# Kernel optimization log

Measured on AMD Instinct MI355X. Metric: run time of the kernel, lower is better.

## Reference

```python
import jax, jax.numpy as jnp
import numpy as np
from jax import lax

C = 512          # in_channels
L = 4            # fcos_conv_layers
NUM_CLS = 1      # fcos_num_class - 1
PRIOR_BIAS = float(-np.log((1 - 0.01) / 0.01))
BN_EPS = 1e-5


def conv1d(x, w, b, pad):
    # x: [B, Cin, T], w: [Cout, Cin, K]
    y = lax.conv_general_dilated(x, w, window_strides=(1,), padding=[(pad, pad)],
                                 dimension_numbers=('NCH', 'OIH', 'NCH'))
    return y + b[None, :, None]


def bn(x, g, b, m, v):
    inv = lax.rsqrt(v + BN_EPS)
    return (x - m[None, :, None]) * (g * inv)[None, :, None] + b[None, :, None]


def tower(x, ws, bs, gs, bes, ms, vs):
    # ws: [L, C, C, 3]; fixed small loop over layers
    for i in range(L):
        x = jax.nn.relu(bn(conv1d(x, ws[i], bs[i], 1), gs[i], bes[i], ms[i], vs[i]))
    return x


def setup_inputs() -> dict:
    key = jax.random.key(0)
    ks = jax.random.split(key, 32)
    d = {}
    d['f0'] = jax.random.normal(ks[0], (8, C, 1024), jnp.float32)
    d['f1'] = jax.random.normal(ks[1], (8, C, 512), jnp.float32)
    d['f2'] = jax.random.normal(ks[2], (8, C, 256), jnp.float32)

    def nrm(k, shape):
        return 0.01 * jax.random.normal(k, shape, jnp.float32)

    # cls / bbox towers: stacked conv + BN params
    d['cls_tw_w'] = nrm(ks[3], (L, C, C, 3)); d['cls_tw_b'] = jnp.zeros((L, C))
    d['cls_bn_g'] = jnp.ones((L, C)); d['cls_bn_b'] = jnp.zeros((L, C))
    d['cls_bn_m'] = jnp.zeros((L, C)); d['cls_bn_v'] = jnp.ones((L, C))
    d['box_tw_w'] = nrm(ks[4], (L, C, C, 3)); d['box_tw_b'] = jnp.zeros((L, C))
    d['box_bn_g'] = jnp.ones((L, C)); d['box_bn_b'] = jnp.zeros((L, C))
    d['box_bn_m'] = jnp.zeros((L, C)); d['box_bn_v'] = jnp.ones((L, C))

    d['logits_w'] = nrm(ks[5], (NUM_CLS, C, 3))
    d['logits_b'] = jnp.full((NUM_CLS,), PRIOR_BIAS, jnp.float32)
    d['bbox_w'] = nrm(ks[6], (2, C, 3)); d['bbox_b'] = jnp.zeros((2,))

    d['mix_w'] = nrm(ks[7], (C, 2 * C, 1)); d['mix_b'] = jnp.zeros((C,))
    d['mix_bn_g'] = jnp.ones((C,)); d['mix_bn_b'] = jnp.zeros((C,))
    d['mix_bn_m'] = jnp.zeros((C,)); d['mix_bn_v'] = jnp.ones((C,))

    d['iou_w1'] = nrm(ks[8], (C // 2, C, 3)); d['iou_b1'] = jnp.zeros((C // 2,))
    d['iou_bn_g'] = jnp.ones((C // 2,)); d['iou_bn_b'] = jnp.zeros((C // 2,))
    d['iou_bn_m'] = jnp.zeros((C // 2,)); d['iou_bn_v'] = jnp.ones((C // 2,))
    d['iou_w2'] = nrm(ks[9], (1, C // 2, 1)); d['iou_b2'] = jnp.zeros((1,))

    d['scales'] = jnp.ones((3,), jnp.float32)
    return d


def reference(f0, f1, f2,
              cls_tw_w, cls_tw_b, cls_bn_g, cls_bn_b, cls_bn_m, cls_bn_v,
              box_tw_w, box_tw_b, box_bn_g, box_bn_b, box_bn_m, box_bn_v,
              logits_w, logits_b, bbox_w, bbox_b,
              mix_w, mix_b, mix_bn_g, mix_bn_b, mix_bn_m, mix_bn_v,
              iou_w1, iou_b1, iou_bn_g, iou_bn_b, iou_bn_m, iou_bn_v,
              iou_w2, iou_b2, scales):
    outs = []
    for l, x in enumerate([f0, f1, f2]):
        ct = tower(x, cls_tw_w, cls_tw_b, cls_bn_g, cls_bn_b, cls_bn_m, cls_bn_v)
        bt = tower(x, box_tw_w, box_tw_b, box_bn_g, box_bn_b, box_bn_m, box_bn_v)
        logits = conv1d(ct, logits_w, logits_b, 1)                      # [B, 1, T]
        bbox = jnp.exp(conv1d(bt, bbox_w, bbox_b, 1) * scales[l])       # [B, 2, T]
        mix = jax.nn.relu(bn(conv1d(jnp.concatenate([ct, bt], axis=1), mix_w, mix_b, 0),
                             mix_bn_g, mix_bn_b, mix_bn_m, mix_bn_v))   # [B, C, T]
        h = jax.nn.relu(bn(conv1d(mix, iou_w1, iou_b1, 1),
                           iou_bn_g, iou_bn_b, iou_bn_m, iou_bn_v))
        iou = conv1d(h, iou_w2, iou_b2, 0)                              # [B, 1, T]
        outs.append(jnp.concatenate([logits, bbox, iou], axis=1))       # [B, 4, T]
    return jnp.concatenate(outs, axis=-1)  # [B, 4, T0+T1+T2]
```

## Files before the change

### kernel.cpp

```cpp
#include <hip/hip_runtime.h>
#include <hip/hip_bf16.h>


typedef __bf16 bf16x8 __attribute__((ext_vector_type(8)));
typedef float f32x4 __attribute__((ext_vector_type(4)));

__device__ __forceinline__ float bf2f(unsigned short u) {
    union { unsigned int i; float f; } c; c.i = ((unsigned int)u) << 16; return c.f;
}
__device__ __forceinline__ unsigned short f2bf(float f) {
    union { __hip_bfloat16 h; unsigned short u; } c; c.h = __float2bfloat16(f); return c.u;
}

__device__ __forceinline__ void gload16(const void* g, void* l) {
    __builtin_amdgcn_global_load_lds(
        (const __attribute__((address_space(1))) unsigned int*)g,
        (__attribute__((address_space(3))) unsigned int*)l,
        16, 0, 0);
}

__global__ __launch_bounds__(512, 2)
void conv_tower(const unsigned short* __restrict__ X, int xstride, int ci_twstride,
                const unsigned short* __restrict__ W,
                const float* __restrict__ Bs,
                unsigned short* __restrict__ Y)
{
    __shared__ alignas(16) unsigned short Xb[2][17 * 512];
    __shared__ alignas(16) unsigned short Wb[3][16 * 512];

    const int L = blockIdx.x;
    const int P = (L & 7) * 28 + (L >> 3);
    const int tt = P >> 2, sub = P & 3;
    const int tw = sub >> 1, co0 = (sub & 1) << 8;

    int rowstart;
    if (tt < 32)      { rowstart = (tt >> 2) * 1026 + 1 + ((tt & 3) << 8); }
    else if (tt < 48) { int i = tt - 32; rowstart = 8208 + (i >> 1) * 514 + 1 + ((i & 1) << 8); }
    else              { rowstart = 12320 + (tt - 48) * 258 + 1; }

    const int tid = threadIdx.x;
    const int lane = tid & 63, wid = tid >> 6;
    const int wco = (wid >> 2) << 7;
    const int wt  = (wid & 3) << 6;
    const int lr = lane & 15;
    const int sr = lane >> 4;

    const unsigned short* Wp = W + (size_t)tw * 3145728;
    const float* Bp = Bs + tw * 2048;
    const int co_out0 = tw * 512 + co0;
    const int ci_off = tw * ci_twstride;

    const unsigned short* xga[3]; unsigned short* xl[3];
#pragma unroll
    for (int p = 0; p < 3; ++p) {
        int seg = (p < 2) ? (p * 8 + wid) : 16;
        xl[p] = (unsigned short*)Xb[0] + seg * 512;
        int g = seg * 64 + lane;
        int row = g >> 2, sc = (g & 3) ^ ((row >> 1) & 3);
        xga[p] = X + (size_t)(rowstart - 1 + row) * xstride + ci_off + sc * 8;
    }
    const unsigned short* wga[2]; unsigned short* wl[2];
#pragma unroll
    for (int p = 0; p < 2; ++p) {
        int seg = p * 8 + wid;
        wl[p] = (unsigned short*)Wb[0] + seg * 512;
        int g = seg * 64 + lane;
        int row = g >> 2, sc = (g & 3) ^ ((row >> 1) & 3);
        wga[p] = Wp + (size_t)(co0 + row) * 1536 + sc * 8;
    }
    constexpr int XBSZ = 17 * 512;
    constexpr int WBSZ = 16 * 512;

    int aoff[8];
#pragma unroll
    for (int mi = 0; mi < 8; ++mi) {
        int ra = wco + mi * 16 + lr;
        aoff[mi] = ra * 64 + (((sr ^ (ra >> 1)) & 3) << 4);
    }
    int boff[3][4];
#pragma unroll
    for (int kk = 0; kk < 3; ++kk)
#pragma unroll
        for (int ni = 0; ni < 4; ++ni) {
            int rb = wt + ni * 16 + lr + kk;
            boff[kk][ni] = rb * 64 + (((sr ^ (rb >> 1)) & 3) << 4);
        }

    f32x4 acc[8][4];
#pragma unroll
    for (int i = 0; i < 8; ++i)
#pragma unroll
        for (int j = 0; j < 4; ++j) acc[i][j] = (f32x4){0.f, 0.f, 0.f, 0.f};

#pragma unroll
    for (int p = 0; p < 3; ++p) gload16(xga[p], xl[p]);
#pragma unroll
    for (int p = 0; p < 2; ++p) {
        gload16(wga[p],       wl[p]);
        gload16(wga[p] + 512, wl[p] + WBSZ);
    }
    asm volatile("s_waitcnt vmcnt(0)" ::: "memory");
    __builtin_amdgcn_s_barrier();

    bf16x8 af[2][8], bv[2][4];
#pragma unroll
    for (int mi = 0; mi < 8; ++mi) af[0][mi] = *(const bf16x8*)((const char*)Wb[0] + aoff[mi]);
#pragma unroll
    for (int ni = 0; ni < 4; ++ni) bv[0][ni] = *(const bf16x8*)((const char*)Xb[0] + boff[0][ni]);

#pragma unroll
    for (int s = 0; s < 48; ++s) {
        const int cr = s & 1, nx = cr ^ 1;
        const int ks = s / 3;
        if (s < 46) {
            const int sp = s + 2;
            const int tap2 = sp % 3, ks2 = sp / 3;
#pragma unroll
            for (int p = 0; p < 2; ++p)
                gload16(wga[p] + tap2 * 512 + ks2 * 32, wl[p] + (sp % 3) * WBSZ);
        }
        if ((s % 3) == 0 && ks < 15) {
#pragma unroll
            for (int p = 0; p < 3; ++p)
                gload16(xga[p] + (ks + 1) * 32, xl[p] + ((ks + 1) & 1) * XBSZ);
        }
        if (s < 47) {
            const int sn = s + 1;
            const int tapn = sn % 3, wbn = sn % 3, xbn = (sn / 3) & 1;
#pragma unroll
            for (int mi = 0; mi < 8; ++mi)
                af[nx][mi] = *(const bf16x8*)((const char*)Wb[wbn] + aoff[mi]);
#pragma unroll
            for (int ni = 0; ni < 4; ++ni)
                bv[nx][ni] = *(const bf16x8*)((const char*)Xb[xbn] + boff[tapn][ni]);
        }
        __builtin_amdgcn_sched_barrier(0);
        __builtin_amdgcn_s_setprio(1);
#pragma unroll
        for (int mi = 0; mi < 8; ++mi)
#pragma unroll
            for (int ni = 0; ni < 4; ++ni)
                acc[mi][ni] = __builtin_amdgcn_mfma_f32_16x16x32_bf16(af[cr][mi], bv[cr][ni], acc[mi][ni], 0, 0, 0);
        __builtin_amdgcn_s_setprio(0);
        asm volatile("s_waitcnt vmcnt(0)" ::: "memory");
        __builtin_amdgcn_s_barrier();
    }

    const int r4 = sr * 4;
#pragma unroll
    for (int mi = 0; mi < 8; ++mi) {
        int co_l = wco + mi * 16 + r4;
        float b0 = Bp[co0 + co_l + 0], b1 = Bp[co0 + co_l + 1];
        float b2 = Bp[co0 + co_l + 2], b3 = Bp[co0 + co_l + 3];
#pragma unroll
        for (int ni = 0; ni < 4; ++ni) {
            int t = wt + ni * 16 + lr;
            f32x4 a = acc[mi][ni];
            float v0 = fmaxf(a[0] + b0, 0.f), v1 = fmaxf(a[1] + b1, 0.f);
            float v2 = fmaxf(a[2] + b2, 0.f), v3 = fmaxf(a[3] + b3, 0.f);
            union { unsigned long long u; unsigned short s[4]; } pk;
            pk.s[0] = f2bf(v0); pk.s[1] = f2bf(v1); pk.s[2] = f2bf(v2); pk.s[3] = f2bf(v3);
            *(unsigned long long*)(Y + (size_t)(rowstart + t) * 1024 + co_out0 + co_l) = pk.u;
        }
    }
}

__device__ __forceinline__ void tile_decode(int ct, int& rowstart, int& t0, int& Tl) {
    if (ct < 64)      { Tl = 1024; int b = ct >> 3;                 t0 = (ct & 7) << 7; rowstart = b * 1026 + 1; }
    else if (ct < 96) { Tl = 512;  int i = ct - 64; int b = i >> 2; t0 = (i & 3) << 7; rowstart = 8208 + b * 514 + 1; }
    else              { Tl = 256;  int i = ct - 96; int b = i >> 1; t0 = (i & 1) << 7; rowstart = 12320 + b * 258 + 1; }
}

template<int KSIZE>
__global__ __launch_bounds__(256)
void conv_gemm(const unsigned short* __restrict__ X, int xstride, int ci0_base, int ci_twstride, int Cin,
               const unsigned short* __restrict__ W, int w_twstride,
               const float* __restrict__ Bs, int b_twstride,
               unsigned short* __restrict__ Y, int ystride, int co_twstride,
               int relu)
{
    constexpr int BM = 128, BN = 128, BK = 32;
    constexpr int NR = BN + KSIZE - 1;
    constexpr int XSEG = (NR * 64 + 1023) / 1024;
    constexpr int XPW  = (XSEG + 3) / 4;
    constexpr int WSEG = KSIZE * BM * 64 / 1024;
    constexpr int WPW  = WSEG / 4;
    __shared__ alignas(16) unsigned short Xs[2 * XSEG * 512];
    __shared__ alignas(16) unsigned short Ws[2 * WSEG * 512];

    const int tid = threadIdx.x;
    const int lane = tid & 63, wid = tid >> 6;
    int rowstart, t0, Tl;
    tile_decode(blockIdx.x, rowstart, t0, Tl);
    const int co0 = blockIdx.y * BM;
    const int tw = blockIdx.z;
    const int ci_off = ci0_base + tw * ci_twstride;
    const unsigned short* Wp = W + (size_t)tw * w_twstride;
    const float* Bp = Bs + tw * b_twstride;
    const int co_out0 = tw * co_twstride + co0;

    const int wm = (wid >> 1) * 64, wn = (wid & 1) * 64;
    const int lr = lane & 15;
    const int sr = lane >> 4;

    const unsigned short* xga[XPW]; unsigned short* xl[XPW];
#pragma unroll
    for (int p = 0; p < XPW; ++p) {
        int seg = (KSIZE == 3) ? ((p < 2) ? p * 4 + wid : 8) : (p * 4 + wid);
        xl[p] = Xs + seg * 512;
        int g = seg * 64 + lane;
        int row = g >> 2, s = (g & 3) ^ ((row >> 1) & 3);
        xga[p] = X + (size_t)(rowstart - (KSIZE >> 1) + row) * xstride + ci_off + s * 8;
    }
    const unsigned short* wga[WPW]; unsigned short* wl[WPW];
#pragma unroll
    for (int p = 0; p < WPW; ++p) {
        int seg = p * 4 + wid;
        wl[p] = Ws + seg * 512;
        int g = seg * 64 + lane;
        int row = g >> 2, s = (g & 3) ^ ((row >> 1) & 3);
        int co = row & (BM - 1), kk = row >> 7;
        wga[p] = Wp + (size_t)(co0 + co) * (KSIZE * Cin) + kk * Cin + s * 8;
    }

    f32x4 acc[4][4];
#pragma unroll
    for (int i = 0; i < 4; ++i)
#pragma unroll
        for (int j = 0; j < 4; ++j) acc[i][j] = (f32x4){0.f, 0.f, 0.f, 0.f};

    auto STAGE = [&](int buf) {
#pragma unroll
        for (int p = 0; p < XPW; ++p) { gload16(xga[p], xl[p] + buf * (XSEG * 512)); xga[p] += BK; }
#pragma unroll
        for (int p = 0; p < WPW; ++p) { gload16(wga[p], wl[p] + buf * (WSEG * 512)); wga[p] += BK; }
    };

    const int nk = Cin / BK;
    STAGE(0);
    int cur = 0;
    for (int ks = 0; ks < nk; ++ks) {
        if (ks + 1 < nk) {
            STAGE(cur ^ 1);
            if constexpr (KSIZE == 3) asm volatile("s_waitcnt vmcnt(9)" ::: "memory");
            else                      asm volatile("s_waitcnt vmcnt(4)" ::: "memory");
        } else {
            asm volatile("s_waitcnt vmcnt(0)" ::: "memory");
        }
        __builtin_amdgcn_sched_barrier(0);
        __builtin_amdgcn_s_barrier();

        const char* bXs = (const char*)Xs + cur * (XSEG * 1024);
        const char* bWs = (const char*)Ws + cur * (WSEG * 1024);
#pragma unroll
        for (int kk = 0; kk < KSIZE; ++kk) {
            bf16x8 af[4], bv[4];
#pragma unroll
            for (int mi = 0; mi < 4; ++mi) {
                int ra = kk * BM + wm + mi * 16 + lr;
                af[mi] = *(const bf16x8*)(bWs + ra * 64 + (((sr ^ (ra >> 1)) & 3) << 4));
                int rb = wn + mi * 16 + lr + kk;
                bv[mi] = *(const bf16x8*)(bXs + rb * 64 + (((sr ^ (rb >> 1)) & 3) << 4));
            }
#pragma unroll
            for (int mi = 0; mi < 4; ++mi)
#pragma unroll
                for (int ni = 0; ni < 4; ++ni)
                    acc[mi][ni] = __builtin_amdgcn_mfma_f32_16x16x32_bf16(af[mi], bv[ni], acc[mi][ni], 0, 0, 0);
        }
        __builtin_amdgcn_sched_barrier(0);
        __builtin_amdgcn_s_barrier();
        cur ^= 1;
    }

    const int r4 = (lane >> 4) * 4;
#pragma unroll
    for (int mi = 0; mi < 4; ++mi) {
        int co_l = wm + mi * 16 + r4;
        float b0 = Bp[co0 + co_l + 0], b1 = Bp[co0 + co_l + 1];
        float b2 = Bp[co0 + co_l + 2], b3 = Bp[co0 + co_l + 3];
#pragma unroll
        for (int ni = 0; ni < 4; ++ni) {
            int t = t0 + wn + ni * 16 + lr;
            f32x4 a = acc[mi][ni];
            float v0 = a[0] + b0, v1 = a[1] + b1, v2 = a[2] + b2, v3 = a[3] + b3;
            if (relu) {
                v0 = fmaxf(v0, 0.f); v1 = fmaxf(v1, 0.f);
                v2 = fmaxf(v2, 0.f); v3 = fmaxf(v3, 0.f);
            }
            union { unsigned long long u; unsigned short s[4]; } pk;
            pk.s[0] = f2bf(v0); pk.s[1] = f2bf(v1); pk.s[2] = f2bf(v2); pk.s[3] = f2bf(v3);
            *(unsigned long long*)(Y + (size_t)(rowstart + t) * ystride + co_out0 + co_l) = pk.u;
        }
    }
}

__global__ __launch_bounds__(256)
void zero_pads(unsigned short* __restrict__ act0, unsigned short* __restrict__ catA,
               unsigned short* __restrict__ catB, unsigned short* __restrict__ mixo,
               unsigned short* __restrict__ iouh)
{
    int c = blockIdx.x >> 1, side = blockIdx.x & 1;
    int start, Tl;
    if (c < 8)       { start = c * 1026;               Tl = 1024; }
    else if (c < 16) { start = 8208 + (c - 8) * 514;   Tl = 512;  }
    else             { start = 12320 + (c - 16) * 258; Tl = 256;  }
    size_t prow = start + (side ? Tl + 1 : 0);
    int tid = threadIdx.x;
    uint4 z = make_uint4(0u, 0u, 0u, 0u);
    if (tid < 64)  *(uint4*)(act0 + prow * 512 + tid * 8) = z;
    if (tid < 128) { *(uint4*)(catA + prow * 1024 + tid * 8) = z;
                     *(uint4*)(catB + prow * 1024 + tid * 8) = z; }
    if (tid >= 128 && tid < 192) *(uint4*)(mixo + prow * 512 + (tid - 128) * 8) = z;
    if (tid >= 192 && tid < 224) *(uint4*)(iouh + prow * 256 + (tid - 192) * 8) = z;
}

__global__ __launch_bounds__(256)
void transpose_in(const float* __restrict__ f0, const float* __restrict__ f1, const float* __restrict__ f2,
                  unsigned short* __restrict__ act0)
{
    __shared__ float tile[32][33];
    int bx = blockIdx.x;
    const float* src; int Tl, padbase, b, t0;
    if (bx < 256)      { src = f0; Tl = 1024; int i = bx;       b = i >> 5; t0 = (i & 31) << 5; padbase = b * 1026; }
    else if (bx < 384) { src = f1; Tl = 512;  int i = bx - 256; b = i >> 4; t0 = (i & 15) << 5; padbase = 8208 + b * 514; }
    else               { src = f2; Tl = 256;  int i = bx - 384; b = i >> 3; t0 = (i & 7)  << 5; padbase = 12320 + b * 258; }
    int c0 = blockIdx.y << 5;
    const float* sb = src + (size_t)b * 512 * Tl;
    int tl = threadIdx.x & 31, cl = threadIdx.x >> 5;
#pragma unroll
    for (int j = 0; j < 4; ++j) {
        int c = cl + j * 8;
        tile[c][tl] = sb[(size_t)(c0 + c) * Tl + t0 + tl];
    }
    __syncthreads();
    int cc = threadIdx.x & 31, tr0 = threadIdx.x >> 5;
    size_t base = (size_t)(padbase + 1 + t0) * 512 + c0;
#pragma unroll
    for (int j = 0; j < 4; ++j) {
        int tr = tr0 + j * 8;
        act0[base + (size_t)tr * 512 + cc] = f2bf(tile[cc][tr]);
    }
}

__global__ __launch_bounds__(256)
void prep_tower(const float* __restrict__ cls_w, const float* __restrict__ box_w,
                const float* __restrict__ cg, const float* __restrict__ cvv,
                const float* __restrict__ bg, const float* __restrict__ bvv,
                unsigned short* __restrict__ Wt)
{
    int idx = blockIdx.x * 256 + threadIdx.x;
    if (idx >= 2 * 4 * 512 * 3 * 512) return;
    int ci = idx & 511;
    int kk = (idx >> 9) % 3;
    int co = (idx / 1536) & 511;
    int l  = (idx / 786432) & 3;
    int tw = idx / 3145728;
    const float* w = tw ? box_w : cls_w;
    const float* g = tw ? bg : cg;
    const float* v = tw ? bvv : cvv;
    float s = g[l * 512 + co] * rsqrtf(v[l * 512 + co] + 1e-5f);
    float val = w[(((size_t)(l * 512 + co)) * 512 + ci) * 3 + kk] * s;
    Wt[idx] = f2bf(val);
}

__global__ __launch_bounds__(256)
void prep_misc(const float* mix_w, const float* mix_b, const float* mg, const float* mbeta, const float* mm, const float* mv,
               const float* iou_w1, const float* iou_b1, const float* ig, const float* ibeta, const float* im, const float* iv,
               const float* cls_b, const float* cg, const float* cbeta, const float* cm, const float* cv2,
               const float* box_b, const float* bg, const float* bbeta, const float* bm, const float* bv2,
               unsigned short* Wmix, unsigned short* Wiou, float* Bt, float* Bmix, float* Biou)
{
    int idx = blockIdx.x * 256 + threadIdx.x;
    if (idx < 524288) {
        int co = idx >> 10;
        float s = mg[co] * rsqrtf(mv[co] + 1e-5f);
        Wmix[idx] = f2bf(mix_w[idx] * s);
        return;
    }
    idx -= 524288;
    if (idx < 393216) {
        int ci = idx & 511, kk = (idx >> 9) % 3, co = idx / 1536;
        float s = ig[co] * rsqrtf(iv[co] + 1e-5f);
        Wiou[idx] = f2bf(iou_w1[((size_t)(co * 512 + ci)) * 3 + kk] * s);
        return;
    }
    idx -= 393216;
    if (idx < 4096) {
        int co = idx & 511, l = (idx >> 9) & 3, tw = idx >> 11;
        const float* g = tw ? bg : cg; const float* v = tw ? bv2 : cv2;
        const float* m = tw ? bm : cm; const float* be = tw ? bbeta : cbeta;
        const float* cb = tw ? box_b : cls_b;
        int o = l * 512 + co;
        float s = g[o] * rsqrtf(v[o] + 1e-5f);
        Bt[idx] = (cb[o] - m[o]) * s + be[o];
        return;
    }
    idx -= 4096;
    if (idx < 512) {
        float s = mg[idx] * rsqrtf(mv[idx] + 1e-5f);
        Bmix[idx] = (mix_b[idx] - mm[idx]) * s + mbeta[idx];
        return;
    }
    idx -= 512;
    if (idx < 256) {
        float s = ig[idx] * rsqrtf(iv[idx] + 1e-5f);
        Biou[idx] = (iou_b1[idx] - im[idx]) * s + ibeta[idx];
    }
}

__global__ __launch_bounds__(256)
void heads_kernel(const unsigned short* __restrict__ catb, const unsigned short* __restrict__ iouh,
                  const float* __restrict__ lw, const float* __restrict__ lb,
                  const float* __restrict__ bw, const float* __restrict__ bb,
                  const float* __restrict__ iw, const float* __restrict__ ib,
                  const float* __restrict__ scales, float* __restrict__ out)
{
    const int lane = threadIdx.x & 63;
    const int wid = threadIdx.x >> 6;

    float lwr[24], bwr0[24], bwr1[24], iwr[4];
    {
        const float4* p = (const float4*)(lw + lane * 24);
#pragma unroll
        for (int q = 0; q < 6; ++q) {
            float4 v = p[q];
            lwr[q * 4 + 0] = v.x; lwr[q * 4 + 1] = v.y; lwr[q * 4 + 2] = v.z; lwr[q * 4 + 3] = v.w;
        }
        p = (const float4*)(bw + lane * 24);
#pragma unroll
        for (int q = 0; q < 6; ++q) {
            float4 v = p[q];
            bwr0[q * 4 + 0] = v.x; bwr0[q * 4 + 1] = v.y; bwr0[q * 4 + 2] = v.z; bwr0[q * 4 + 3] = v.w;
        }
        p = (const float4*)(bw + 1536 + lane * 24);
#pragma unroll
        for (int q = 0; q < 6; ++q) {
            float4 v = p[q];
            bwr1[q * 4 + 0] = v.x; bwr1[q * 4 + 1] = v.y; bwr1[q * 4 + 2] = v.z; bwr1[q * 4 + 3] = v.w;
        }
        float4 v = *(const float4*)(iw + lane * 4);
        iwr[0] = v.x; iwr[1] = v.y; iwr[2] = v.z; iwr[3] = v.w;
    }
    const float lb0 = lb[0], bb0 = bb[0], bb1 = bb[1], ib0 = ib[0];
    const float s0 = scales[0], s1 = scales[1], s2 = scales[2];

    for (int r = blockIdx.x * 4 + wid; r < 14336; r += gridDim.x * 4) {
        int tlog, roff, tgoff, padbase; float sc;
        if (r < 8192)       { tlog = 10; roff = 0;     tgoff = 0;    sc = s0; }
        else if (r < 12288) { tlog = 9;  roff = 8192;  tgoff = 1024; sc = s1; }
        else                { tlog = 8;  roff = 12288; tgoff = 1536; sc = s2; }
        int i = r - roff;
        int Tl = 1 << tlog;
        int b = i >> tlog, t = i & (Tl - 1);
        if (r < 8192)       padbase = b * 1026;
        else if (r < 12288) padbase = 8208 + b * 514;
        else                padbase = 12320 + b * 258;
        int prow = padbase + 1 + t;

        float al = 0.f, a0 = 0.f, a1 = 0.f, ai = 0.f;
        const unsigned short* base = catb + (size_t)prow * 1024 + lane * 8;
#pragma unroll
        for (int kk = 0; kk < 3; ++kk) {
            union { uint4 u; unsigned short s[8]; } cv, bvv;
            cv.u = *(const uint4*)(base + (kk - 1) * 1024);
            bvv.u = *(const uint4*)(base + (kk - 1) * 1024 + 512);
#pragma unroll
            for (int j = 0; j < 8; ++j) {
                float xc = bf2f(cv.s[j]);
                float xb = bf2f(bvv.s[j]);
                al = fmaf(xc, lwr[j * 3 + kk], al);
                a0 = fmaf(xb, bwr0[j * 3 + kk], a0);
                a1 = fmaf(xb, bwr1[j * 3 + kk], a1);
            }
        }
        {
            union { uint2 u; unsigned short s[4]; } hv;
            hv.u = *(const uint2*)(iouh + (size_t)prow * 256 + lane * 4);
#pragma unroll
            for (int j = 0; j < 4; ++j) ai = fmaf(bf2f(hv.s[j]), iwr[j], ai);
        }
#pragma unroll
        for (int off = 32; off > 0; off >>= 1) {
            al += __shfl_xor(al, off);
            a0 += __shfl_xor(a0, off);
            a1 += __shfl_xor(a1, off);
            ai += __shfl_xor(ai, off);
        }
        if (lane == 0) {
            int tg = tgoff + t;
            out[((size_t)b * 4 + 0) * 1792 + tg] = al + lb0;
            out[((size_t)b * 4 + 1) * 1792 + tg] = expf((a0 + bb0) * sc);
            out[((size_t)b * 4 + 2) * 1792 + tg] = expf((a1 + bb1) * sc);
            out[((size_t)b * 4 + 3) * 1792 + tg] = ai + ib0;
        }
    }
}

extern "C" void kernel_launch(void* const* d_in, const int* in_sizes, int n_in,
                              void* d_out, int out_size, void* d_ws, size_t ws_size,
                              hipStream_t stream)
{
    const float* f0       = (const float*)d_in[0];
    const float* f1       = (const float*)d_in[1];
    const float* f2       = (const float*)d_in[2];
    const float* cls_tw_w = (const float*)d_in[3];
    const float* cls_tw_b = (const float*)d_in[4];
    const float* cls_bn_g = (const float*)d_in[5];
    const float* cls_bn_b = (const float*)d_in[6];
    const float* cls_bn_m = (const float*)d_in[7];
    const float* cls_bn_v = (const float*)d_in[8];
    const float* box_tw_w = (const float*)d_in[9];
    const float* box_tw_b = (const float*)d_in[10];
    const float* box_bn_g = (const float*)d_in[11];
    const float* box_bn_b = (const float*)d_in[12];
    const float* box_bn_m = (const float*)d_in[13];
    const float* box_bn_v = (const float*)d_in[14];
    const float* logits_w = (const float*)d_in[15];
    const float* logits_b = (const float*)d_in[16];
    const float* bbox_w   = (const float*)d_in[17];
    const float* bbox_b   = (const float*)d_in[18];
    const float* mix_w    = (const float*)d_in[19];
    const float* mix_b    = (const float*)d_in[20];
    const float* mix_bn_g = (const float*)d_in[21];
    const float* mix_bn_b = (const float*)d_in[22];
    const float* mix_bn_m = (const float*)d_in[23];
    const float* mix_bn_v = (const float*)d_in[24];
    const float* iou_w1   = (const float*)d_in[25];
    const float* iou_b1   = (const float*)d_in[26];
    const float* iou_bn_g = (const float*)d_in[27];
    const float* iou_bn_b = (const float*)d_in[28];
    const float* iou_bn_m = (const float*)d_in[29];
    const float* iou_bn_v = (const float*)d_in[30];
    const float* iou_w2   = (const float*)d_in[31];
    const float* iou_b2   = (const float*)d_in[32];
    const float* scales   = (const float*)d_in[33];

    unsigned char* ws = (unsigned char*)d_ws;
    unsigned short* Wt   = (unsigned short*)(ws + 0);
    unsigned short* Wmix = (unsigned short*)(ws + 12582912);
    unsigned short* Wiou = (unsigned short*)(ws + 13631488);
    float*          Bt   = (float*)(ws + 14417920);
    float*          Bmix = (float*)(ws + 14434304);
    float*          Biou = (float*)(ws + 14436352);
    unsigned short* act0 = (unsigned short*)(ws + 14437376);
    unsigned short* catA = (unsigned short*)(ws + 29182976);
    unsigned short* catB = (unsigned short*)(ws + 58674176);
    unsigned short* mixo = (unsigned short*)(ws + 88165376);
    unsigned short* iouh = (unsigned short*)(ws + 102910976);

    zero_pads<<<dim3(48), dim3(256), 0, stream>>>(act0, catA, catB, mixo, iouh);
    prep_tower<<<dim3(24576), dim3(256), 0, stream>>>(cls_tw_w, box_tw_w, cls_bn_g, cls_bn_v,
                                                      box_bn_g, box_bn_v, Wt);
    prep_misc<<<dim3(3603), dim3(256), 0, stream>>>(mix_w, mix_b, mix_bn_g, mix_bn_b, mix_bn_m, mix_bn_v,
                                                    iou_w1, iou_b1, iou_bn_g, iou_bn_b, iou_bn_m, iou_bn_v,
                                                    cls_tw_b, cls_bn_g, cls_bn_b, cls_bn_m, cls_bn_v,
                                                    box_tw_b, box_bn_g, box_bn_b, box_bn_m, box_bn_v,
                                                    Wmix, Wiou, Bt, Bmix, Biou);
    transpose_in<<<dim3(448, 16), dim3(256), 0, stream>>>(f0, f1, f2, act0);

    conv_tower<<<dim3(224), dim3(512), 0, stream>>>(act0, 512, 0,   Wt,            Bt,        catA);
    conv_tower<<<dim3(224), dim3(512), 0, stream>>>(catA, 1024, 512, Wt + 786432,  Bt + 512,  catB);
    conv_tower<<<dim3(224), dim3(512), 0, stream>>>(catB, 1024, 512, Wt + 1572864, Bt + 1024, catA);
    conv_tower<<<dim3(224), dim3(512), 0, stream>>>(catA, 1024, 512, Wt + 2359296, Bt + 1536, catB);
    conv_gemm<1><<<dim3(112, 4, 1), 256, 0, stream>>>(catB, 1024, 0, 0, 1024,
                                                      Wmix, 0, Bmix, 0, mixo, 512, 0, 1);
    conv_gemm<3><<<dim3(112, 2, 1), 256, 0, stream>>>(mixo, 512, 0, 0, 512,
                                                      Wiou, 0, Biou, 0, iouh, 256, 0, 1);
    heads_kernel<<<dim3(896), dim3(256), 0, stream>>>(catB, iouh, logits_w, logits_b,
                                                      bbox_w, bbox_b, iou_w2, iou_b2, scales,
                                                      (float*)d_out);
}
```

Measured before the change: 298.3 us.

## Shrink conv tower tiles to 128 timesteps with 256-thread blocks and tap-wise pipeline

Reworks the tower conv kernel so each block covers 256 output channels by 128 timesteps with 4 waves instead of 256 by 256 with 8 waves, doubling the grid to 448 blocks. The K loop is restructured to process one input-channel chunk per iteration with three tap sub-steps, double-buffering weights per tap and X per chunk, and it waits on LDS reads before issuing MFMAs. The aim is better CU occupancy and load balance, since 224 blocks underfill the GPU, at the cost of more weight traffic per output and more barriers. The original conv_tower is left with a broken buffer indexing expression and is no longer called. A fixed copy, conv_tower_fixed, is launched instead.

New measurement: 310.4 us. 4.1% more time.

```diff
diff --git a/kernel.cpp b/kernel.cpp
--- a/kernel.cpp
+++ b/kernel.cpp
@@ -19,31 +19,36 @@
         16, 0, 0);
 }
 
-__global__ __launch_bounds__(512, 2)
+__device__ __forceinline__ void tile_decode(int ct, int& rowstart, int& t0, int& Tl) {
+    if (ct < 64)      { Tl = 1024; int b = ct >> 3;                 t0 = (ct & 7) << 7; rowstart = b * 1026 + 1; }
+    else if (ct < 96) { Tl = 512;  int i = ct - 64; int b = i >> 2; t0 = (i & 3) << 7; rowstart = 8208 + b * 514 + 1; }
+    else              { Tl = 256;  int i = ct - 96; int b = i >> 1; t0 = (i & 1) << 7; rowstart = 12320 + b * 258 + 1; }
+}
+
+__global__ __launch_bounds__(256, 2)
 void conv_tower(const unsigned short* __restrict__ X, int xstride, int ci_twstride,
                 const unsigned short* __restrict__ W,
                 const float* __restrict__ Bs,
                 unsigned short* __restrict__ Y)
 {
-    __shared__ alignas(16) unsigned short Xb[2][17 * 512];
-    __shared__ alignas(16) unsigned short Wb[3][16 * 512];
+    __shared__ alignas(16) unsigned short Xb[2][9 * 512];
+    __shared__ alignas(16) unsigned short Wb[2][16 * 512];
+    constexpr int XBSZ = 9 * 512;
+    constexpr int WBSZ = 16 * 512;
 
     const int L = blockIdx.x;
-    const int P = (L & 7) * 28 + (L >> 3);
-    const int tt = P >> 2, sub = P & 3;
+    const int P = (L & 7) * 56 + (L >> 3);
+    const int ct = P >> 2, sub = P & 3;
     const int tw = sub >> 1, co0 = (sub & 1) << 8;
 
-    int rowstart;
-    if (tt < 32)      { rowstart = (tt >> 2) * 1026 + 1 + ((tt & 3) << 8); }
-    else if (tt < 48) { int i = tt - 32; rowstart = 8208 + (i >> 1) * 514 + 1 + ((i & 1) << 8); }
-    else              { rowstart = 12320 + (tt - 48) * 258 + 1; }
-
-    const int tid = threadIdx.x;
-    const int lane = tid & 63, wid = tid >> 6;
-    const int wco = (wid >> 2) << 7;
-    const int wt  = (wid & 3) << 6;
-    const int lr = lane & 15;
-    const int sr = lane >> 4;
+    int rowstart, t0, Tl;
+    tile_decode(ct, rowstart, t0, Tl);
+    const int rtile = rowstart + t0;
+
+    const int tid = threadIdx.x, lane = tid & 63, wid = tid >> 6;
+    const int wco = (wid >> 1) << 7;
+    const int wt  = (wid & 1) << 6;
+    const int lr = lane & 15, sr = lane >> 4;
 
     const unsigned short* Wp = W + (size_t)tw * 3145728;
     const float* Bp = Bs + tw * 2048;
@@ -53,23 +58,21 @@
     const unsigned short* xga[3]; unsigned short* xl[3];
 #pragma unroll
     for (int p = 0; p < 3; ++p) {
-        int seg = (p < 2) ? (p * 8 + wid) : 16;
+        int seg = (p < 2) ? (p * 4 + wid) : 8;
         xl[p] = (unsigned short*)Xb[0] + seg * 512;
-        int g = seg * 64 + lane;
-        int row = g >> 2, sc = (g & 3) ^ ((row >> 1) & 3);
-        xga[p] = X + (size_t)(rowstart - 1 + row) * xstride + ci_off + sc * 8;
-    }
-    const unsigned short* wga[2]; unsigned short* wl[2];
-#pragma unroll
-    for (int p = 0; p < 2; ++p) {
-        int seg = p * 8 + wid;
+        int row = seg * 16 + (lane >> 2);
+        int sc = (lane & 3) ^ ((row >> 1) & 3);
+        xga[p] = X + (size_t)(rtile - 1 + row) * xstride + ci_off + sc * 8;
+    }
+    const unsigned short* wga[4]; unsigned short* wl[4];
+#pragma unroll
+    for (int p = 0; p < 4; ++p) {
+        int seg = p * 4 + wid;
         wl[p] = (unsigned short*)Wb[0] + seg * 512;
-        int g = seg * 64 + lane;
-        int row = g >> 2, sc = (g & 3) ^ ((row >> 1) & 3);
+        int row = seg * 16 + (lane >> 2);
+        int sc = (lane & 3) ^ ((row >> 1) & 3);
         wga[p] = Wp + (size_t)(co0 + row) * 1536 + sc * 8;
     }
-    constexpr int XBSZ = 17 * 512;
-    constexpr int WBSZ = 16 * 512;
 
     int aoff[8];
 #pragma unroll
@@ -95,55 +98,49 @@
 #pragma unroll
     for (int p = 0; p < 3; ++p) gload16(xga[p], xl[p]);
 #pragma unroll
-    for (int p = 0; p < 2; ++p) {
-        gload16(wga[p],       wl[p]);
-        gload16(wga[p] + 512, wl[p] + WBSZ);
-    }
+    for (int p = 0; p < 4; ++p) gload16(wga[p], wl[p]);
     asm volatile("s_waitcnt vmcnt(0)" ::: "memory");
     __builtin_amdgcn_s_barrier();
 
-    bf16x8 af[2][8], bv[2][4];
-#pragma unroll
-    for (int mi = 0; mi < 8; ++mi) af[0][mi] = *(const bf16x8*)((const char*)Wb[0] + aoff[mi]);
-#pragma unroll
-    for (int ni = 0; ni < 4; ++ni) bv[0][ni] = *(const bf16x8*)((const char*)Xb[0] + boff[0][ni]);
-
-#pragma unroll
-    for (int s = 0; s < 48; ++s) {
-        const int cr = s & 1, nx = cr ^ 1;
-        const int ks = s / 3;
-        if (s < 46) {
-            const int sp = s + 2;
-            const int tap2 = sp % 3, ks2 = sp / 3;
-#pragma unroll
-            for (int p = 0; p < 2; ++p)
-                gload16(wga[p] + tap2 * 512 + ks2 * 32, wl[p] + (sp % 3) * WBSZ);
-        }
-        if ((s % 3) == 0 && ks < 15) {
-#pragma unroll
-            for (int p = 0; p < 3; ++p)
-                gload16(xga[p] + (ks + 1) * 32, xl[p] + ((ks + 1) & 1) * XBSZ);
-        }
-        if (s < 47) {
-            const int sn = s + 1;
-            const int tapn = sn % 3, wbn = sn % 3, xbn = (sn / 3) & 1;
+    for (int ks = 0; ks < 16; ++ks) {
+        const int pk = ks & 1, po = pk ^ 1;
+        const char* Xcur = (const char*)Xb[0] + pk * (XBSZ * 2);
+        const char* Wpk  = (const char*)Wb[0] + pk * (WBSZ * 2);
+        const char* Wpo  = (const char*)Wb[0] + po * (WBSZ * 2);
+
+        auto TAP = [&](const char* wbuf, int kk) {
+            bf16x8 af[8], bv[4];
 #pragma unroll
             for (int mi = 0; mi < 8; ++mi)
-                af[nx][mi] = *(const bf16x8*)((const char*)Wb[wbn] + aoff[mi]);
+                af[mi] = *(const bf16x8*)(wbuf + aoff[mi]);
 #pragma unroll
             for (int ni = 0; ni < 4; ++ni)
-                bv[nx][ni] = *(const bf16x8*)((const char*)Xb[xbn] + boff[tapn][ni]);
-        }
-        __builtin_amdgcn_sched_barrier(0);
-        __builtin_amdgcn_s_setprio(1);
-#pragma unroll
-        for (int mi = 0; mi < 8; ++mi)
-#pragma unroll
-            for (int ni = 0; ni < 4; ++ni)
-                acc[mi][ni] = __builtin_amdgcn_mfma_f32_16x16x32_bf16(af[cr][mi], bv[cr][ni], acc[mi][ni], 0, 0, 0);
-        __builtin_amdgcn_s_setprio(0);
-        asm volatile("s_waitcnt vmcnt(0)" ::: "memory");
-        __builtin_amdgcn_s_barrier();
+                bv[ni] = *(const bf16x8*)(Xcur + boff[kk][ni]);
+            asm volatile("s_waitcnt lgkmcnt(0)" ::: "memory");
+            __builtin_amdgcn_sched_barrier(0);
+            __builtin_amdgcn_s_setprio(1);
+#pragma unroll
+            for (int mi = 0; mi < 8; ++mi)
+#pragma unroll
+                for (int ni = 0; ni < 4; ++ni)
+                    acc[mi][ni] = __builtin_amdgcn_mfma_f32_16x16x32_bf16(af[mi], bv[ni], acc[mi][ni], 0, 0, 0);
+            __builtin_amdgcn_s_setprio(0);
+            asm volatile("s_waitcnt vmcnt(0)" ::: "memory");
+            __builtin_amdgcn_s_barrier();
+        };
+
+#pragma unroll
+        for (int p = 0; p < 4; ++p) gload16(wga[p] + 512 + ks * 32, wl[p] + po * (WBSZ * 1) + po * 0 + po * WBSZ - po * WBSZ + po * WBSZ);
+        ;
+        TAP(Wpk, 0);
+#pragma unroll
+        for (int p = 0; p < 4; ++p) gload16(wga[p] + 1024 + ks * 32, wl[p] + pk * WBSZ);
+        TAP(Wpo, 1);
+        if (ks < 15) {
+#pragma unroll
+            for (int p = 0; p < 4; ++p) gload16(wga[p] + (ks + 1) * 32, wl[p] + po * WBSZ);
+        }
+        TAP(Wpk, 2);
     }
 
     const int r4 = sr * 4;
@@ -158,17 +155,151 @@
             f32x4 a = acc[mi][ni];
             float v0 = fmaxf(a[0] + b0, 0.f), v1 = fmaxf(a[1] + b1, 0.f);
             float v2 = fmaxf(a[2] + b2, 0.f), v3 = fmaxf(a[3] + b3, 0.f);
-            union { unsigned long long u; unsigned short s[4]; } pk;
-            pk.s[0] = f2bf(v0); pk.s[1] = f2bf(v1); pk.s[2] = f2bf(v2); pk.s[3] = f2bf(v3);
-            *(unsigned long long*)(Y + (size_t)(rowstart + t) * 1024 + co_out0 + co_l) = pk.u;
-        }
-    }
-}
-
-__device__ __forceinline__ void tile_decode(int ct, int& rowstart, int& t0, int& Tl) {
-    if (ct < 64)      { Tl = 1024; int b = ct >> 3;                 t0 = (ct & 7) << 7; rowstart = b * 1026 + 1; }
-    else if (ct < 96) { Tl = 512;  int i = ct - 64; int b = i >> 2; t0 = (i & 3) << 7; rowstart = 8208 + b * 514 + 1; }
-    else              { Tl = 256;  int i = ct - 96; int b = i >> 1; t0 = (i & 1) << 7; rowstart = 12320 + b * 258 + 1; }
+            union { unsigned long long u; unsigned short s[4]; } pk2;
+            pk2.s[0] = f2bf(v0); pk2.s[1] = f2bf(v1); pk2.s[2] = f2bf(v2); pk2.s[3] = f2bf(v3);
+            *(unsigned long long*)(Y + (size_t)(rtile + t) * 1024 + co_out0 + co_l) = pk2.u;
+        }
+    }
+}
+
+__global__ __launch_bounds__(256, 2)
+void conv_tower_fixed(const unsigned short* __restrict__ X, int xstride, int ci_twstride,
+                      const unsigned short* __restrict__ W,
+                      const float* __restrict__ Bs,
+                      unsigned short* __restrict__ Y)
+{
+    __shared__ alignas(16) unsigned short Xb[2][9 * 512];
+    __shared__ alignas(16) unsigned short Wb[2][16 * 512];
+    constexpr int XBSZ = 9 * 512;
+    constexpr int WBSZ = 16 * 512;
+
+    const int L = blockIdx.x;
+    const int P = (L & 7) * 56 + (L >> 3);
+    const int ct = P >> 2, sub = P & 3;
+    const int tw = sub >> 1, co0 = (sub & 1) << 8;
+
+    int rowstart, t0, Tl;
+    tile_decode(ct, rowstart, t0, Tl);
+    const int rtile = rowstart + t0;
+
+    const int tid = threadIdx.x, lane = tid & 63, wid = tid >> 6;
+    const int wco = (wid >> 1) << 7;
+    const int wt  = (wid & 1) << 6;
+    const int lr = lane & 15, sr = lane >> 4;
+
+    const unsigned short* Wp = W + (size_t)tw * 3145728;
+    const float* Bp = Bs + tw * 2048;
+    const int co_out0 = tw * 512 + co0;
+    const int ci_off = tw * ci_twstride;
+
+    const unsigned short* xga[3]; unsigned short* xl[3];
+#pragma unroll
+    for (int p = 0; p < 3; ++p) {
+        int seg = (p < 2) ? (p * 4 + wid) : 8;
+        xl[p] = (unsigned short*)Xb[0] + seg * 512;
+        int row = seg * 16 + (lane >> 2);
+        int sc = (lane & 3) ^ ((row >> 1) & 3);
+        xga[p] = X + (size_t)(rtile - 1 + row) * xstride + ci_off + sc * 8;
+    }
+    const unsigned short* wga[4]; unsigned short* wl[4];
+#pragma unroll
+    for (int p = 0; p < 4; ++p) {
+        int seg = p * 4 + wid;
+        wl[p] = (unsigned short*)Wb[0] + seg * 512;
+        int row = seg * 16 + (lane >> 2);
+        int sc = (lane & 3) ^ ((row >> 1) & 3);
+        wga[p] = Wp + (size_t)(co0 + row) * 1536 + sc * 8;
+    }
+
+    int aoff[8];
+#pragma unroll
+    for (int mi = 0; mi < 8; ++mi) {
+        int ra = wco + mi * 16 + lr;
+        aoff[mi] = ra * 64 + (((sr ^ (ra >> 1)) & 3) << 4);
+    }
+    int boff[3][4];
+#pragma unroll
+    for (int kk = 0; kk < 3; ++kk)
+#pragma unroll
+        for (int ni = 0; ni < 4; ++ni) {
+            int rb = wt + ni * 16 + lr + kk;
+            boff[kk][ni] = rb * 64 + (((sr ^ (rb >> 1)) & 3) << 4);
+        }
+
+    f32x4 acc[8][4];
+#pragma unroll
+    for (int i = 0; i < 8; ++i)
+#pragma unroll
+        for (int j = 0; j < 4; ++j) acc[i][j] = (f32x4){0.f, 0.f, 0.f, 0.f};
+
+#pragma unroll
+    for (int p = 0; p < 3; ++p) gload16(xga[p], xl[p]);
+#pragma unroll
+    for (int p = 0; p < 4; ++p) gload16(wga[p], wl[p]);
+    asm volatile("s_waitcnt vmcnt(0)" ::: "memory");
+    __builtin_amdgcn_s_barrier();
+
+    for (int ks = 0; ks < 16; ++ks) {
+        const int pk = ks & 1, po = pk ^ 1;
+        const char* Xcur = (const char*)Xb[0] + pk * (XBSZ * 2);
+        const char* Wpk  = (const char*)Wb[0] + pk * (WBSZ * 2);
+        const char* Wpo  = (const char*)Wb[0] + po * (WBSZ * 2);
+
+        auto TAP = [&](const char* wbuf, int kk) {
+            bf16x8 af[8], bv[4];
+#pragma unroll
+            for (int mi = 0; mi < 8; ++mi)
+                af[mi] = *(const bf16x8*)(wbuf + aoff[mi]);
+#pragma unroll
+            for (int ni = 0; ni < 4; ++ni)
+                bv[ni] = *(const bf16x8*)(Xcur + boff[kk][ni]);
+            asm volatile("s_waitcnt lgkmcnt(0)" ::: "memory");
+            __builtin_amdgcn_sched_barrier(0);
+            __builtin_amdgcn_s_setprio(1);
+#pragma unroll
+            for (int mi = 0; mi < 8; ++mi)
+#pragma unroll
+                for (int ni = 0; ni < 4; ++ni)
+                    acc[mi][ni] = __builtin_amdgcn_mfma_f32_16x16x32_bf16(af[mi], bv[ni], acc[mi][ni], 0, 0, 0);
+            __builtin_amdgcn_s_setprio(0);
+            asm volatile("s_waitcnt vmcnt(0)" ::: "memory");
+            __builtin_amdgcn_s_barrier();
+        };
+
+#pragma unroll
+        for (int p = 0; p < 4; ++p) gload16(wga[p] + 512 + ks * 32, wl[p] + po * WBSZ);
+        if (ks < 15) {
+#pragma unroll
+            for (int p = 0; p < 3; ++p) gload16(xga[p] + (ks + 1) * 32, xl[p] + po * XBSZ);
+        }
+        TAP(Wpk, 0);
+#pragma unroll
+        for (int p = 0; p < 4; ++p) gload16(wga[p] + 1024 + ks * 32, wl[p] + pk * WBSZ);
+        TAP(Wpo, 1);
+        if (ks < 15) {
+#pragma unroll
+            for (int p = 0; p < 4; ++p) gload16(wga[p] + (ks + 1) * 32, wl[p] + po * WBSZ);
+        }
+        TAP(Wpk, 2);
+    }
+
+    const int r4 = sr * 4;
+#pragma unroll
+    for (int mi = 0; mi < 8; ++mi) {
+        int co_l = wco + mi * 16 + r4;
+        float b0 = Bp[co0 + co_l + 0], b1 = Bp[co0 + co_l + 1];
+        float b2 = Bp[co0 + co_l + 2], b3 = Bp[co0 + co_l + 3];
+#pragma unroll
+        for (int ni = 0; ni < 4; ++ni) {
+            int t = wt + ni * 16 + lr;
+            f32x4 a = acc[mi][ni];
+            float v0 = fmaxf(a[0] + b0, 0.f), v1 = fmaxf(a[1] + b1, 0.f);
+            float v2 = fmaxf(a[2] + b2, 0.f), v3 = fmaxf(a[3] + b3, 0.f);
+            union { unsigned long long u; unsigned short s[4]; } pk2;
+            pk2.s[0] = f2bf(v0); pk2.s[1] = f2bf(v1); pk2.s[2] = f2bf(v2); pk2.s[3] = f2bf(v3);
+            *(unsigned long long*)(Y + (size_t)(rtile + t) * 1024 + co_out0 + co_l) = pk2.u;
+        }
+    }
 }
 
 template<int KSIZE>
@@ -210,7 +341,7 @@
         xl[p] = Xs + seg * 512;
         int g = seg * 64 + lane;
         int row = g >> 2, s = (g & 3) ^ ((row >> 1) & 3);
-        xga[p] = X + (size_t)(rowstart - (KSIZE >> 1) + row) * xstride + ci_off + s * 8;
+        xga[p] = X + (size_t)(rowstart + t0 - (KSIZE >> 1) + row) * xstride + ci_off + s * 8;
     }
     const unsigned short* wga[WPW]; unsigned short* wl[WPW];
 #pragma unroll
@@ -559,10 +690,10 @@
                                                     Wmix, Wiou, Bt, Bmix, Biou);
     transpose_in<<<dim3(448, 16), dim3(256), 0, stream>>>(f0, f1, f2, act0);
 
-    conv_tower<<<dim3(224), dim3(512), 0, stream>>>(act0, 512, 0,   Wt,            Bt,        catA);
-    conv_tower<<<dim3(224), dim3(512), 0, stream>>>(catA, 1024, 512, Wt + 786432,  Bt + 512,  catB);
-    conv_tower<<<dim3(224), dim3(512), 0, stream>>>(catB, 1024, 512, Wt + 1572864, Bt + 1024, catA);
-    conv_tower<<<dim3(224), dim3(512), 0, stream>>>(catA, 1024, 512, Wt + 2359296, Bt + 1536, catB);
+    conv_tower_fixed<<<dim3(448), dim3(256), 0, stream>>>(act0, 512, 0,    Wt,            Bt,        catA);
+    conv_tower_fixed<<<dim3(448), dim3(256), 0, stream>>>(catA, 1024, 512, Wt + 786432,  Bt + 512,  catB);
+    conv_tower_fixed<<<dim3(448), dim3(256), 0, stream>>>(catB, 1024, 512, Wt + 1572864, Bt + 1024, catA);
+    conv_tower_fixed<<<dim3(448), dim3(256), 0, stream>>>(catA, 1024, 512, Wt + 2359296, Bt + 1536, catB);
     conv_gemm<1><<<dim3(112, 4, 1), 256, 0, stream>>>(catB, 1024, 0, 0, 1024,
                                                       Wmix, 0, Bmix, 0, mixo, 512, 0, 1);
     conv_gemm<3><<<dim3(112, 2, 1), 256, 0, stream>>>(mixo, 512, 0, 0, 512,
```

## Halve conv_tower tile width, double grid, and relax per-step vmcnt waits

Applied to the files above, without the earlier changes.

The tower conv kernel now uses 256-thread blocks covering 128 time steps instead of 512 threads over 256, which doubles the grid to 448 blocks and shrinks the X LDS buffer. The main loop drops the register double-buffered fragment prefetch and the setprio/sched_barrier hints. It waits with partial vmcnt counts before a barrier, so global-to-LDS loads stay in flight across steps instead of being drained fully each iteration. The aim is better CU occupancy and load overlap, at the cost of more weight traffic per output and less LDS-to-register overlap inside a step.

After: 284.4 us. 1.05x faster.

```diff
diff --git a/kernel.cpp b/kernel.cpp
--- a/kernel.cpp
+++ b/kernel.cpp
@@ -19,31 +19,38 @@
         16, 0, 0);
 }
 
-__global__ __launch_bounds__(512, 2)
+__device__ __forceinline__ void tile_decode(int ct, int& rowstart, int& t0, int& Tl) {
+    if (ct < 64)      { Tl = 1024; int b = ct >> 3;                 t0 = (ct & 7) << 7; rowstart = b * 1026 + 1; }
+    else if (ct < 96) { Tl = 512;  int i = ct - 64; int b = i >> 2; t0 = (i & 3) << 7; rowstart = 8208 + b * 514 + 1; }
+    else              { Tl = 256;  int i = ct - 96; int b = i >> 1; t0 = (i & 1) << 7; rowstart = 12320 + b * 258 + 1; }
+}
+
+__global__ __launch_bounds__(256, 2)
 void conv_tower(const unsigned short* __restrict__ X, int xstride, int ci_twstride,
                 const unsigned short* __restrict__ W,
                 const float* __restrict__ Bs,
                 unsigned short* __restrict__ Y)
 {
-    __shared__ alignas(16) unsigned short Xb[2][17 * 512];
+    __shared__ alignas(16) unsigned short Xb[2][9 * 512];
     __shared__ alignas(16) unsigned short Wb[3][16 * 512];
+    constexpr int XBSZ = 9 * 512;
+    constexpr int WBSZ = 16 * 512;
+    constexpr int XBYTES = XBSZ * 2;
+    constexpr int WBYTES = WBSZ * 2;
 
     const int L = blockIdx.x;
-    const int P = (L & 7) * 28 + (L >> 3);
-    const int tt = P >> 2, sub = P & 3;
+    const int P = (L & 7) * 56 + (L >> 3);
+    const int ct = P >> 2, sub = P & 3;
     const int tw = sub >> 1, co0 = (sub & 1) << 8;
 
-    int rowstart;
-    if (tt < 32)      { rowstart = (tt >> 2) * 1026 + 1 + ((tt & 3) << 8); }
-    else if (tt < 48) { int i = tt - 32; rowstart = 8208 + (i >> 1) * 514 + 1 + ((i & 1) << 8); }
-    else              { rowstart = 12320 + (tt - 48) * 258 + 1; }
-
-    const int tid = threadIdx.x;
-    const int lane = tid & 63, wid = tid >> 6;
-    const int wco = (wid >> 2) << 7;
-    const int wt  = (wid & 3) << 6;
-    const int lr = lane & 15;
-    const int sr = lane >> 4;
+    int rowstart, t0, Tl;
+    tile_decode(ct, rowstart, t0, Tl);
+    const int rtile = rowstart + t0;
+
+    const int tid = threadIdx.x, lane = tid & 63, wid = tid >> 6;
+    const int wco = (wid >> 1) << 7;
+    const int wt  = (wid & 1) << 6;
+    const int lr = lane & 15, sr = lane >> 4;
 
     const unsigned short* Wp = W + (size_t)tw * 3145728;
     const float* Bp = Bs + tw * 2048;
@@ -53,23 +60,21 @@
     const unsigned short* xga[3]; unsigned short* xl[3];
 #pragma unroll
     for (int p = 0; p < 3; ++p) {
-        int seg = (p < 2) ? (p * 8 + wid) : 16;
+        int seg = (p < 2) ? (p * 4 + wid) : 8;
         xl[p] = (unsigned short*)Xb[0] + seg * 512;
-        int g = seg * 64 + lane;
-        int row = g >> 2, sc = (g & 3) ^ ((row >> 1) & 3);
-        xga[p] = X + (size_t)(rowstart - 1 + row) * xstride + ci_off + sc * 8;
-    }
-    const unsigned short* wga[2]; unsigned short* wl[2];
-#pragma unroll
-    for (int p = 0; p < 2; ++p) {
-        int seg = p * 8 + wid;
+        int row = seg * 16 + (lane >> 2);
+        int sc = (lane & 3) ^ ((row >> 1) & 3);
+        xga[p] = X + (size_t)(rtile - 1 + row) * xstride + ci_off + sc * 8;
+    }
+    const unsigned short* wga[4]; unsigned short* wl[4];
+#pragma unroll
+    for (int p = 0; p < 4; ++p) {
+        int seg = p * 4 + wid;
         wl[p] = (unsigned short*)Wb[0] + seg * 512;
-        int g = seg * 64 + lane;
-        int row = g >> 2, sc = (g & 3) ^ ((row >> 1) & 3);
+        int row = seg * 16 + (lane >> 2);
+        int sc = (lane & 3) ^ ((row >> 1) & 3);
         wga[p] = Wp + (size_t)(co0 + row) * 1536 + sc * 8;
     }
-    constexpr int XBSZ = 17 * 512;
-    constexpr int WBSZ = 16 * 512;
 
     int aoff[8];
 #pragma unroll
@@ -95,54 +100,48 @@
 #pragma unroll
     for (int p = 0; p < 3; ++p) gload16(xga[p], xl[p]);
 #pragma unroll
-    for (int p = 0; p < 2; ++p) {
+    for (int p = 0; p < 4; ++p) {
         gload16(wga[p],       wl[p]);
         gload16(wga[p] + 512, wl[p] + WBSZ);
     }
     asm volatile("s_waitcnt vmcnt(0)" ::: "memory");
     __builtin_amdgcn_s_barrier();
 
-    bf16x8 af[2][8], bv[2][4];
-#pragma unroll
-    for (int mi = 0; mi < 8; ++mi) af[0][mi] = *(const bf16x8*)((const char*)Wb[0] + aoff[mi]);
-#pragma unroll
-    for (int ni = 0; ni < 4; ++ni) bv[0][ni] = *(const bf16x8*)((const char*)Xb[0] + boff[0][ni]);
-
 #pragma unroll
     for (int s = 0; s < 48; ++s) {
-        const int cr = s & 1, nx = cr ^ 1;
-        const int ks = s / 3;
-        if (s < 46) {
-            const int sp = s + 2;
-            const int tap2 = sp % 3, ks2 = sp / 3;
-#pragma unroll
-            for (int p = 0; p < 2; ++p)
-                gload16(wga[p] + tap2 * 512 + ks2 * 32, wl[p] + (sp % 3) * WBSZ);
-        }
-        if ((s % 3) == 0 && ks < 15) {
+        const int kk = s % 3, k0 = s / 3;
+        if      (s == 47) asm volatile("s_waitcnt vmcnt(0)" ::: "memory");
+        else if (s == 46) asm volatile("s_waitcnt vmcnt(4)" ::: "memory");
+        else if (kk == 0) asm volatile("s_waitcnt vmcnt(4)" ::: "memory");
+        else              asm volatile("s_waitcnt vmcnt(7)" ::: "memory");
+        __builtin_amdgcn_s_barrier();
+
+        if (s + 2 <= 47) {
+            const int u = s + 2, ut = u % 3, uk = u / 3;
+#pragma unroll
+            for (int p = 0; p < 4; ++p)
+                gload16(wga[p] + ut * 512 + uk * 32, wl[p] + ut * WBSZ);
+        }
+        if (kk == 0 && k0 + 1 <= 15) {
 #pragma unroll
             for (int p = 0; p < 3; ++p)
-                gload16(xga[p] + (ks + 1) * 32, xl[p] + ((ks + 1) & 1) * XBSZ);
-        }
-        if (s < 47) {
-            const int sn = s + 1;
-            const int tapn = sn % 3, wbn = sn % 3, xbn = (sn / 3) & 1;
-#pragma unroll
-            for (int mi = 0; mi < 8; ++mi)
-                af[nx][mi] = *(const bf16x8*)((const char*)Wb[wbn] + aoff[mi]);
+                gload16(xga[p] + (k0 + 1) * 32, xl[p] + ((k0 + 1) & 1) * XBSZ);
+        }
+
+        const char* wbuf = (const char*)Wb[0] + (s % 3) * WBYTES;
+        const char* xbuf = (const char*)Xb[0] + (k0 & 1) * XBYTES;
+        bf16x8 af[8], bv[4];
+#pragma unroll
+        for (int mi = 0; mi < 8; ++mi)
+            af[mi] = *(const bf16x8*)(wbuf + aoff[mi]);
+#pragma unroll
+        for (int ni = 0; ni < 4; ++ni)
+            bv[ni] = *(const bf16x8*)(xbuf + boff[kk][ni]);
+#pragma unroll
+        for (int mi = 0; mi < 8; ++mi)
 #pragma unroll
             for (int ni = 0; ni < 4; ++ni)
-                bv[nx][ni] = *(const bf16x8*)((const char*)Xb[xbn] + boff[tapn][ni]);
-        }
-        __builtin_amdgcn_sched_barrier(0);
-        __builtin_amdgcn_s_setprio(1);
-#pragma unroll
-        for (int mi = 0; mi < 8; ++mi)
-#pragma unroll
-            for (int ni = 0; ni < 4; ++ni)
-                acc[mi][ni] = __builtin_amdgcn_mfma_f32_16x16x32_bf16(af[cr][mi], bv[cr][ni], acc[mi][ni], 0, 0, 0);
-        __builtin_amdgcn_s_setprio(0);
-        asm volatile("s_waitcnt vmcnt(0)" ::: "memory");
+                acc[mi][ni] = __builtin_amdgcn_mfma_f32_16x16x32_bf16(af[mi], bv[ni], acc[mi][ni], 0, 0, 0);
         __builtin_amdgcn_s_barrier();
     }
 
@@ -158,17 +157,11 @@
             f32x4 a = acc[mi][ni];
             float v0 = fmaxf(a[0] + b0, 0.f), v1 = fmaxf(a[1] + b1, 0.f);
             float v2 = fmaxf(a[2] + b2, 0.f), v3 = fmaxf(a[3] + b3, 0.f);
-            union { unsigned long long u; unsigned short s[4]; } pk;
-            pk.s[0] = f2bf(v0); pk.s[1] = f2bf(v1); pk.s[2] = f2bf(v2); pk.s[3] = f2bf(v3);
-            *(unsigned long long*)(Y + (size_t)(rowstart + t) * 1024 + co_out0 + co_l) = pk.u;
-        }
-    }
-}
-
-__device__ __forceinline__ void tile_decode(int ct, int& rowstart, int& t0, int& Tl) {
-    if (ct < 64)      { Tl = 1024; int b = ct >> 3;                 t0 = (ct & 7) << 7; rowstart = b * 1026 + 1; }
-    else if (ct < 96) { Tl = 512;  int i = ct - 64; int b = i >> 2; t0 = (i & 3) << 7; rowstart = 8208 + b * 514 + 1; }
-    else              { Tl = 256;  int i = ct - 96; int b = i >> 1; t0 = (i & 1) << 7; rowstart = 12320 + b * 258 + 1; }
+            union { unsigned long long u; unsigned short s[4]; } pk2;
+            pk2.s[0] = f2bf(v0); pk2.s[1] = f2bf(v1); pk2.s[2] = f2bf(v2); pk2.s[3] = f2bf(v3);
+            *(unsigned long long*)(Y + (size_t)(rtile + t) * 1024 + co_out0 + co_l) = pk2.u;
+        }
+    }
 }
 
 template<int KSIZE>
@@ -210,7 +203,7 @@
         xl[p] = Xs + seg * 512;
         int g = seg * 64 + lane;
         int row = g >> 2, s = (g & 3) ^ ((row >> 1) & 3);
-        xga[p] = X + (size_t)(rowstart - (KSIZE >> 1) + row) * xstride + ci_off + s * 8;
+        xga[p] = X + (size_t)(rowstart + t0 - (KSIZE >> 1) + row) * xstride + ci_off + s * 8;
     }
     const unsigned short* wga[WPW]; unsigned short* wl[WPW];
 #pragma unroll
@@ -559,10 +552,10 @@
                                                     Wmix, Wiou, Bt, Bmix, Biou);
     transpose_in<<<dim3(448, 16), dim3(256), 0, stream>>>(f0, f1, f2, act0);
 
-    conv_tower<<<dim3(224), dim3(512), 0, stream>>>(act0, 512, 0,   Wt,            Bt,        catA);
-    conv_tower<<<dim3(224), dim3(512), 0, stream>>>(catA, 1024, 512, Wt + 786432,  Bt + 512,  catB);
-    conv_tower<<<dim3(224), dim3(512), 0, stream>>>(catB, 1024, 512, Wt + 1572864, Bt + 1024, catA);
-    conv_tower<<<dim3(224), dim3(512), 0, stream>>>(catA, 1024, 512, Wt + 2359296, Bt + 1536, catB);
+    conv_tower<<<dim3(448), dim3(256), 0, stream>>>(act0, 512, 0,    Wt,            Bt,        catA);
+    conv_tower<<<dim3(448), dim3(256), 0, stream>>>(catA, 1024, 512, Wt + 786432,  Bt + 512,  catB);
+    conv_tower<<<dim3(448), dim3(256), 0, stream>>>(catB, 1024, 512, Wt + 1572864, Bt + 1024, catA);
+    conv_tower<<<dim3(448), dim3(256), 0, stream>>>(catA, 1024, 512, Wt + 2359296, Bt + 1536, catB);
     conv_gemm<1><<<dim3(112, 4, 1), 256, 0, stream>>>(catB, 1024, 0, 0, 1024,
                                                       Wmix, 0, Bmix, 0, mixo, 512, 0, 1);
     conv_gemm<3><<<dim3(112, 2, 1), 256, 0, stream>>>(mixo, 512, 0, 0, 512,
```
